# Kernel tuning notes

Measured on AMD Instinct MI355X. Metric: run time of the kernel, lower is better.

Reference implementation:

```python
import jax, jax.numpy as jnp
import numpy as np

NUM_HEADS = 16
D_IN = 1024
D_OUT = 64  # = D_IN // NUM_HEADS
N = 2048


def setup_inputs() -> dict:
    key = jax.random.key(0)
    kx, kq, kk, kv, ko = jax.random.split(key, 5)
    x = jax.random.normal(kx, (N, D_IN), dtype=jnp.float32)
    # per-head projection weights, stacked over heads (torch code keeps a
    # Python list of SelfAttention modules; stacking is the vectorized form)
    q_proj = jax.random.normal(kq, (NUM_HEADS, D_IN, D_OUT), dtype=jnp.float32)
    k_proj = jax.random.normal(kk, (NUM_HEADS, D_IN, D_OUT), dtype=jnp.float32)
    v_proj = jax.random.normal(kv, (NUM_HEADS, D_IN, D_OUT), dtype=jnp.float32)
    o_proj = jax.random.normal(ko, (D_IN, D_IN), dtype=jnp.float32)
    return {"x": x, "q_proj": q_proj, "k_proj": k_proj, "v_proj": v_proj, "o_proj": o_proj}


def reference(x, q_proj, k_proj, v_proj, o_proj):
    d_out = q_proj.shape[-1]
    # per-head projections: [H, N, E]
    q = jnp.einsum('nd,hde->hne', x, q_proj)
    k = jnp.einsum('nd,hde->hne', x, k_proj)
    v = jnp.einsum('nd,hde->hne', x, v_proj)
    # full NxN scores per head (matches the naive torch implementation's math)
    scores = jnp.einsum('hne,hme->hnm', q, k) / jnp.sqrt(jnp.float32(d_out))
    attn = jax.nn.softmax(scores, axis=-1)
    ctx = jnp.einsum('hnm,hme->hne', attn, v)
    # concat heads along the feature dim (head 0 first, as in torch.cat)
    h, n, e = ctx.shape
    out = jnp.transpose(ctx, (1, 0, 2)).reshape(n, h * e)
    return out @ o_proj
```

## Files before the change

kernel.cpp:

```cpp
#include <hip/hip_runtime.h>

#define H 16
#define N 2048
#define E 64
#define D 1024

typedef __attribute__((ext_vector_type(8))) short bf16x8;
typedef __attribute__((ext_vector_type(4))) float f32x4;

__device__ __forceinline__ float bf2f(unsigned short u) {
    union { unsigned int i; float f; } v;
    v.i = ((unsigned int)u) << 16;
    return v.f;
}
__device__ __forceinline__ unsigned short f2bf(float f) {
    unsigned int u = __float_as_uint(f);
    return (unsigned short)((u + 0x7fffu + ((u >> 16) & 1u)) >> 16);
}
#define MFMA(a, b, c) __builtin_amdgcn_mfma_f32_16x16x32_bf16(a, b, c, 0, 0, 0)

typedef __attribute__((address_space(3))) unsigned int lds_u32;
typedef const __attribute__((address_space(1))) unsigned int glb_u32;
__device__ __forceinline__ void dma16(const unsigned short* g, unsigned short* l) {
    __builtin_amdgcn_global_load_lds((glb_u32*)g, (lds_u32*)l, 16, 0, 0);
}

__device__ __forceinline__ int sw8(int row, int c)  { return row * 64  + ((c ^ (row & 7)) << 3); }
__device__ __forceinline__ int sw16(int row, int c) { return row * 128 + ((c ^ (row & 7)) << 3); }
__device__ __forceinline__ int swp(int row, int c)  { return row * 128 + ((c ^ (row & 15)) << 3); }

__global__ __launch_bounds__(256) void convert_all_kernel(
    const float* __restrict__ x,
    const float* __restrict__ qw, const float* __restrict__ kw,
    const float* __restrict__ vw, const float* __restrict__ ow,
    unsigned short* __restrict__ xh, unsigned short* __restrict__ xl,
    unsigned short* __restrict__ wBh, unsigned short* __restrict__ wBl,
    unsigned short* __restrict__ wvt, unsigned short* __restrict__ woh)
{
    __shared__ float ts[64][65];
    const int b0 = blockIdx.x;
    const int t = threadIdx.x;
    if (b0 < 2048) {
        const int i = (b0 * 256 + t) * 4;
        const float4 v = *(const float4*)&x[i];
        ushort4 hh, ll;
        hh.x = f2bf(v.x); ll.x = f2bf(v.x - bf2f(hh.x));
        hh.y = f2bf(v.y); ll.y = f2bf(v.y - bf2f(hh.y));
        hh.z = f2bf(v.z); ll.z = f2bf(v.z - bf2f(hh.z));
        hh.w = f2bf(v.w); ll.w = f2bf(v.w - bf2f(hh.w));
        *(ushort4*)&xh[i] = hh;
        *(ushort4*)&xl[i] = ll;
        return;
    }
    const int b = b0 - 2048;
    const float* src;
    int rs, dt, orow0;
    bool has_lo;
    unsigned short *dh, *dl;
    if (b < 768) {
        const int which = b >> 8, r = b & 255, h = r >> 4;
        dt = r & 15;
        src = (which == 0 ? qw : which == 1 ? kw : vw) + ((size_t)h * D + dt * 64) * E;
        rs = E;
        if (which == 0)      { dh = wBh; dl = wBl; orow0 = h * 64;        has_lo = true; }
        else if (which == 1) { dh = wBh; dl = wBl; orow0 = 1024 + h * 64; has_lo = true; }
        else                 { dh = wvt; dl = wBl; orow0 = h * 64;        has_lo = false; }
    } else {
        const int r = b - 768, ct = r >> 4;
        dt = r & 15;
        src = ow + (size_t)(dt * 64) * D + ct * 64;
        rs = D;
        orow0 = ct * 64;
        dh = woh; dl = wBl; has_lo = false;
    }
    {
        const int row = t >> 2, cb = (t & 3) * 16;
        #pragma unroll
        for (int j = 0; j < 16; j += 4) {
            const float4 v = *(const float4*)&src[row * rs + cb + j];
            ts[row][cb + j + 0] = v.x;
            ts[row][cb + j + 1] = v.y;
            ts[row][cb + j + 2] = v.z;
            ts[row][cb + j + 3] = v.w;
        }
    }
    __syncthreads();
    {
        const int cl = t >> 2, dp = (t & 3) * 16;
        bf16x8 hv0, hv1, lv0, lv1;
        #pragma unroll
        for (int i = 0; i < 16; ++i) {
            const float f = ts[dp + i][cl];
            const unsigned short hh = f2bf(f);
            const unsigned short lo = f2bf(f - bf2f(hh));
            if (i < 8) { hv0[i] = (short)hh; lv0[i] = (short)lo; }
            else       { hv1[i - 8] = (short)hh; lv1[i - 8] = (short)lo; }
        }
        const size_t o = (size_t)(orow0 + cl) * D + dt * 64 + dp;
        *(bf16x8*)&dh[o] = hv0;
        *(bf16x8*)&dh[o + 8] = hv1;
        if (has_lo) {
            *(bf16x8*)&dl[o] = lv0;
            *(bf16x8*)&dl[o + 8] = lv1;
        }
    }
}

__global__ __launch_bounds__(256, 3) void qkv_kernel(
    const unsigned short* __restrict__ xh, const unsigned short* __restrict__ xl,
    const unsigned short* __restrict__ wBh, const unsigned short* __restrict__ wBl,
    const unsigned short* __restrict__ wvt,
    unsigned short* __restrict__ Qh, unsigned short* __restrict__ Ql,
    unsigned short* __restrict__ Kh, unsigned short* __restrict__ Kl,
    unsigned short* __restrict__ Vt)
{
    __shared__ unsigned short ash[128 * 64], asl[128 * 64];
    __shared__ unsigned short bsh[64 * 64], bsl[64 * 64];
    const int n0 = blockIdx.x * 128;
    const int ct0 = blockIdx.y;
    const int sec = ct0 >> 4;
    const int hh = ct0 & 15;
    const bool isv = (sec == 2);
    const unsigned short* Bh = isv ? wvt : wBh;
    const size_t brow0 = (sec == 1 ? 1024 : 0) + hh * 64;

    const int t = threadIdx.x;
    const int lane = t & 63, wvi = t >> 6, quad = lane >> 4, l15 = lane & 15;

    f32x4 acc[2][4];
    #pragma unroll
    for (int i = 0; i < 2; ++i)
        #pragma unroll
        for (int j = 0; j < 4; ++j) acc[i][j] = (f32x4){0.f, 0.f, 0.f, 0.f};

    for (int k0 = 0; k0 < D; k0 += 64) {
        __syncthreads();
        #pragma unroll
        for (int p = 0; p < 4; ++p) {
            const int row = p * 32 + wvi * 8 + (lane >> 3);
            const int lc = (lane & 7) ^ (row & 7);
            const int lo = p * 2048 + wvi * 512 + lane * 8;
            const size_t ga = (size_t)(n0 + row) * D + k0 + lc * 8;
            dma16(&xh[ga], &ash[lo]);
            if (!isv) dma16(&xl[ga], &asl[lo]);
        }
        #pragma unroll
        for (int p = 0; p < 2; ++p) {
            const int row = p * 32 + wvi * 8 + (lane >> 3);
            const int lc = (lane & 7) ^ (row & 7);
            const int lo = p * 2048 + wvi * 512 + lane * 8;
            const size_t gb = (brow0 + row) * D + k0 + lc * 8;
            dma16(&Bh[gb], &bsh[lo]);
            if (!isv) dma16(&wBl[gb], &bsl[lo]);
        }
        __syncthreads();

        #pragma unroll
        for (int kwi = 0; kwi < 2; ++kwi) {
            const int c = kwi * 4 + quad;
            bf16x8 ah[2], al[2], bh[4], bl[4];
            #pragma unroll
            for (int i = 0; i < 2; ++i) {
                ah[i] = *(const bf16x8*)&ash[sw8(wvi * 32 + i * 16 + l15, c)];
                if (!isv) al[i] = *(const bf16x8*)&asl[sw8(wvi * 32 + i * 16 + l15, c)];
            }
            #pragma unroll
            for (int j = 0; j < 4; ++j) {
                bh[j] = *(const bf16x8*)&bsh[sw8(j * 16 + l15, c)];
                if (!isv) bl[j] = *(const bf16x8*)&bsl[sw8(j * 16 + l15, c)];
            }
            #pragma unroll
            for (int i = 0; i < 2; ++i)
                #pragma unroll
                for (int j = 0; j < 4; ++j) {
                    acc[i][j] = MFMA(ah[i], bh[j], acc[i][j]);
                    if (!isv) {
                        acc[i][j] = MFMA(ah[i], bl[j], acc[i][j]);
                        acc[i][j] = MFMA(al[i], bh[j], acc[i][j]);
                    }
                }
        }
    }

    if (isv) {
        #pragma unroll
        for (int j = 0; j < 4; ++j) {
            const int e = j * 16 + l15;
            #pragma unroll
            for (int i = 0; i < 2; ++i) {
                const int nb = n0 + wvi * 32 + i * 16 + quad * 4;
                ushort4 pk;
                pk.x = f2bf(acc[i][j][0]);
                pk.y = f2bf(acc[i][j][1]);
                pk.z = f2bf(acc[i][j][2]);
                pk.w = f2bf(acc[i][j][3]);
                *(ushort4*)&Vt[((size_t)hh * 64 + e) * N + nb] = pk;
            }
        }
    } else {
        const float scale = (sec == 0) ? 0.125f : 1.0f;
        unsigned short* Oh = (sec == 0) ? Qh : Kh;
        unsigned short* Ol = (sec == 0) ? Ql : Kl;
        #pragma unroll
        for (int j = 0; j < 4; ++j) {
            const int e = j * 16 + l15;
            #pragma unroll
            for (int i = 0; i < 2; ++i)
                #pragma unroll
                for (int r = 0; r < 4; ++r) {
                    const int n = n0 + wvi * 32 + i * 16 + quad * 4 + r;
                    const float val = acc[i][j][r] * scale;
                    const unsigned short hv = f2bf(val);
                    Oh[((size_t)hh * N + n) * E + e] = hv;
                    Ol[((size_t)hh * N + n) * E + e] = f2bf(val - bf2f(hv));
                }
        }
    }
}

__global__ __launch_bounds__(256, 2) void attn_kernel(
    const unsigned short* __restrict__ Qh, const unsigned short* __restrict__ Ql,
    const unsigned short* __restrict__ Kh, const unsigned short* __restrict__ Kl,
    const unsigned short* __restrict__ Vt,
    unsigned short* __restrict__ Op0, unsigned short* __restrict__ Op1,
    float* __restrict__ mlp)
{
    __shared__ unsigned short kbuf[2 * 16384];
    __shared__ unsigned short vts[64 * 128];
    const int r0 = blockIdx.x * 128, h = blockIdx.y, split = blockIdx.z;
    const int mb = split * 1024;
    const int t = threadIdx.x, lane = t & 63, wvi = t >> 6, quad = lane >> 4, l15 = lane & 15;

    bf16x8 qfh[2][2], qfl[2][2];
    #pragma unroll
    for (int i = 0; i < 2; ++i) {
        const size_t base = ((size_t)h * N + r0 + wvi * 32 + i * 16 + l15) * E;
        #pragma unroll
        for (int kwi = 0; kwi < 2; ++kwi) {
            qfh[i][kwi] = *(const bf16x8*)&Qh[base + kwi * 32 + quad * 8];
            qfl[i][kwi] = *(const bf16x8*)&Ql[base + kwi * 32 + quad * 8];
        }
    }

    f32x4 oacc[2][4];
    float mrow[2][4], lrow[2][4];
    #pragma unroll
    for (int i = 0; i < 2; ++i)
        #pragma unroll
        for (int j = 0; j < 4; ++j) {
            oacc[i][j] = (f32x4){0.f, 0.f, 0.f, 0.f};
            mrow[i][j] = -1e30f;
            lrow[i][j] = 0.f;
        }

    #pragma unroll
    for (int p = 0; p < 4; ++p) {
        const int row = p * 32 + wvi * 8 + (lane >> 3);
        const int lc = (lane & 7) ^ (row & 7);
        const int lo = p * 2048 + wvi * 512 + lane * 8;
        const size_t gk = ((size_t)h * N + mb + row) * E + lc * 8;
        dma16(&Kh[gk], &kbuf[lo]);
        dma16(&Kl[gk], &kbuf[8192 + lo]);
    }

    for (int it = 0; it < 8; ++it) {
        const int cur = it & 1;
        __syncthreads();

        #pragma unroll
        for (int p = 0; p < 4; ++p) {
            const int row = p * 16 + wvi * 4 + (lane >> 4);
            const int lc = (lane & 15) ^ (row & 7);
            const int lo = p * 2048 + wvi * 512 + lane * 8;
            dma16(&Vt[((size_t)h * 64 + row) * N + mb + it * 128 + lc * 8], &vts[lo]);
        }

        const unsigned short* ksh = &kbuf[cur * 16384];
        const unsigned short* ksl = ksh + 8192;

        f32x4 s[2][8];
        #pragma unroll
        for (int i = 0; i < 2; ++i)
            #pragma unroll
            for (int ct = 0; ct < 8; ++ct) s[i][ct] = (f32x4){0.f, 0.f, 0.f, 0.f};

        #pragma unroll
        for (int kwi = 0; kwi < 2; ++kwi) {
            const int c = kwi * 4 + quad;
            #pragma unroll
            for (int ct = 0; ct < 8; ++ct) {
                const bf16x8 bh = *(const bf16x8*)&ksh[sw8(ct * 16 + l15, c)];
                const bf16x8 bl = *(const bf16x8*)&ksl[sw8(ct * 16 + l15, c)];
                #pragma unroll
                for (int i = 0; i < 2; ++i) {
                    s[i][ct] = MFMA(qfh[i][kwi], bh, s[i][ct]);
                    s[i][ct] = MFMA(qfh[i][kwi], bl, s[i][ct]);
                    s[i][ct] = MFMA(qfl[i][kwi], bh, s[i][ct]);
                }
            }
        }

        #pragma unroll
        for (int i = 0; i < 2; ++i)
            #pragma unroll
            for (int r = 0; r < 4; ++r) {
                float mx = s[i][0][r];
                #pragma unroll
                for (int ct = 1; ct < 8; ++ct) mx = fmaxf(mx, s[i][ct][r]);
                mx = fmaxf(mx, __shfl_xor(mx, 1));
                mx = fmaxf(mx, __shfl_xor(mx, 2));
                mx = fmaxf(mx, __shfl_xor(mx, 4));
                mx = fmaxf(mx, __shfl_xor(mx, 8));
                const float mn = fmaxf(mrow[i][r], mx);
                const float alpha = __expf(mrow[i][r] - mn);
                mrow[i][r] = mn;
                float sum = 0.f;
                #pragma unroll
                for (int ct = 0; ct < 8; ++ct) {
                    const float p = __expf(s[i][ct][r] - mn);
                    s[i][ct][r] = p;
                    sum += p;
                }
                sum += __shfl_xor(sum, 1);
                sum += __shfl_xor(sum, 2);
                sum += __shfl_xor(sum, 4);
                sum += __shfl_xor(sum, 8);
                lrow[i][r] = lrow[i][r] * alpha + sum;
                #pragma unroll
                for (int ct = 0; ct < 4; ++ct) oacc[i][ct][r] *= alpha;
            }

        __syncthreads();

        if (it < 7) {
            #pragma unroll
            for (int p = 0; p < 4; ++p) {
                const int row = p * 32 + wvi * 8 + (lane >> 3);
                const int lc = (lane & 7) ^ (row & 7);
                const int lo = (cur ^ 1) * 16384 + p * 2048 + wvi * 512 + lane * 8;
                const size_t gk = ((size_t)h * N + mb + (it + 1) * 128 + row) * E + lc * 8;
                dma16(&Kh[gk], &kbuf[lo]);
                dma16(&Kl[gk], &kbuf[8192 + lo]);
            }
        }

        unsigned short* ps = &kbuf[cur * 16384];
        #pragma unroll
        for (int i = 0; i < 2; ++i)
            #pragma unroll
            for (int ct = 0; ct < 8; ++ct)
                #pragma unroll
                for (int r = 0; r < 4; ++r) {
                    const int row = wvi * 32 + i * 16 + quad * 4 + r;
                    const int chunk = ct * 2 + (l15 >> 3);
                    ps[swp(row, chunk) + (l15 & 7)] = f2bf(s[i][ct][r]);
                }

        #pragma unroll
        for (int kwi = 0; kwi < 4; ++kwi) {
            bf16x8 vb[4];
            #pragma unroll
            for (int ct = 0; ct < 4; ++ct)
                vb[ct] = *(const bf16x8*)&vts[sw16(ct * 16 + l15, kwi * 4 + quad)];
            #pragma unroll
            for (int i = 0; i < 2; ++i) {
                const int prow = wvi * 32 + i * 16 + l15;
                const bf16x8 pa = *(const bf16x8*)&ps[swp(prow, kwi * 4 + quad)];
                #pragma unroll
                for (int ct = 0; ct < 4; ++ct)
                    oacc[i][ct] = MFMA(pa, vb[ct], oacc[i][ct]);
            }
        }
    }

    unsigned short* Opc = split ? Op1 : Op0;
    #pragma unroll
    for (int i = 0; i < 2; ++i)
        #pragma unroll
        for (int r = 0; r < 4; ++r) {
            const int n = r0 + wvi * 32 + i * 16 + quad * 4 + r;
            if (l15 == 0) {
                mlp[(((size_t)split * 16 + h) * 2048 + n) * 2 + 0] = mrow[i][r];
                mlp[(((size_t)split * 16 + h) * 2048 + n) * 2 + 1] = lrow[i][r];
            }
            #pragma unroll
            for (int ct = 0; ct < 4; ++ct)
                Opc[((size_t)h * 2048 + n) * 64 + ct * 16 + l15] = f2bf(oacc[i][ct][r]);
        }
}

__global__ __launch_bounds__(256) void combine_kernel(
    const unsigned short* __restrict__ Op0, const unsigned short* __restrict__ Op1,
    const float* __restrict__ mlp, unsigned short* __restrict__ Ch)
{
    const int h = blockIdx.y;
    const int n = blockIdx.x * 64 + (threadIdx.x >> 2);
    const int e0 = (threadIdx.x & 3) * 16;
    const float m0 = mlp[((size_t)h * 2048 + n) * 2 + 0];
    const float l0 = mlp[((size_t)h * 2048 + n) * 2 + 1];
    const float m1 = mlp[((size_t)(16 + h) * 2048 + n) * 2 + 0];
    const float l1 = mlp[((size_t)(16 + h) * 2048 + n) * 2 + 1];
    const float M = fmaxf(m0, m1);
    const float a0 = __expf(m0 - M), a1 = __expf(m1 - M);
    const float inv = 1.f / (l0 * a0 + l1 * a1);
    const size_t ib = ((size_t)h * 2048 + n) * 64 + e0;
    const size_t ob = (size_t)n * D + h * 64 + e0;
    #pragma unroll
    for (int j = 0; j < 2; ++j) {
        const bf16x8 v0 = *(const bf16x8*)&Op0[ib + j * 8];
        const bf16x8 v1 = *(const bf16x8*)&Op1[ib + j * 8];
        bf16x8 o;
        #pragma unroll
        for (int k = 0; k < 8; ++k) {
            const float c = (bf2f((unsigned short)v0[k]) * a0 +
                             bf2f((unsigned short)v1[k]) * a1) * inv;
            o[k] = (short)f2bf(c);
        }
        *(bf16x8*)&Ch[ob + j * 8] = o;
    }
}

__global__ __launch_bounds__(256, 4) void out_proj_kernel(
    const unsigned short* __restrict__ Chh, const unsigned short* __restrict__ Wh,
    float* __restrict__ out)
{
    __shared__ unsigned short ash[64 * 64], bsh[64 * 64];
    const int n0 = blockIdx.x * 64, c0 = blockIdx.y * 64;
    const int t = threadIdx.x, lane = t & 63, wvi = t >> 6, quad = lane >> 4, l15 = lane & 15;

    f32x4 acc[4];
    #pragma unroll
    for (int j = 0; j < 4; ++j) acc[j] = (f32x4){0.f, 0.f, 0.f, 0.f};

    for (int k0 = 0; k0 < D; k0 += 64) {
        __syncthreads();
        #pragma unroll
        for (int p = 0; p < 2; ++p) {
            const int row = p * 32 + wvi * 8 + (lane >> 3);
            const int lc = (lane & 7) ^ (row & 7);
            const int lo = p * 2048 + wvi * 512 + lane * 8;
            dma16(&Chh[(size_t)(n0 + row) * D + k0 + lc * 8], &ash[lo]);
            dma16(&Wh[(size_t)(c0 + row) * D + k0 + lc * 8], &bsh[lo]);
        }
        __syncthreads();

        #pragma unroll
        for (int kwi = 0; kwi < 2; ++kwi) {
            const int c = kwi * 4 + quad;
            const bf16x8 ah = *(const bf16x8*)&ash[sw8(wvi * 16 + l15, c)];
            #pragma unroll
            for (int j = 0; j < 4; ++j) {
                const bf16x8 bh = *(const bf16x8*)&bsh[sw8(j * 16 + l15, c)];
                acc[j] = MFMA(ah, bh, acc[j]);
            }
        }
    }

    #pragma unroll
    for (int r = 0; r < 4; ++r) {
        const int n = n0 + wvi * 16 + quad * 4 + r;
        #pragma unroll
        for (int j = 0; j < 4; ++j)
            out[(size_t)n * D + c0 + j * 16 + l15] = acc[j][r];
    }
}

extern "C" void kernel_launch(void* const* d_in, const int* in_sizes, int n_in,
                              void* d_out, int out_size, void* d_ws, size_t ws_size,
                              hipStream_t stream) {
    const float* x  = (const float*)d_in[0];
    const float* qw = (const float*)d_in[1];
    const float* kw = (const float*)d_in[2];
    const float* vw = (const float*)d_in[3];
    const float* ow = (const float*)d_in[4];
    float* out = (float*)d_out;

    unsigned short* ws = (unsigned short*)d_ws;
    const size_t M1 = 1024 * 1024;
    unsigned short* wBh = ws;
    unsigned short* wBl = ws + 2 * M1;
    unsigned short* wvt = ws + 4 * M1;
    unsigned short* woh = ws + 5 * M1;
    unsigned short* xh  = ws + 6 * M1;
    unsigned short* xl  = ws + 8 * M1;
    unsigned short* Qh  = ws + 10 * M1;
    unsigned short* Ql  = ws + 12 * M1;
    unsigned short* Kh  = ws + 14 * M1;
    unsigned short* Kl  = ws + 16 * M1;
    unsigned short* Vt  = ws + 18 * M1;
    unsigned short* Ch  = xh;

    unsigned short* Op0 = wBh;
    unsigned short* Op1 = wBl;
    float* mlp = (float*)wvt;

    convert_all_kernel<<<3072, 256, 0, stream>>>(x, qw, kw, vw, ow,
                                                 xh, xl, wBh, wBl, wvt, woh);
    qkv_kernel<<<dim3(16, 48), 256, 0, stream>>>(xh, xl, wBh, wBl, wvt,
                                                 Qh, Ql, Kh, Kl, Vt);
    attn_kernel<<<dim3(16, 16, 2), 256, 0, stream>>>(Qh, Ql, Kh, Kl, Vt,
                                                     Op0, Op1, mlp);
    combine_kernel<<<dim3(32, 16), 256, 0, stream>>>(Op0, Op1, mlp, Ch);
    out_proj_kernel<<<dim3(32, 16), 256, 0, stream>>>(Ch, woh, out);
}
```

Baseline: 181.2 us.

## Transpose score MFMA so P stays in registers for PV product

Swaps MFMA operand order so the score tile comes out transposed, with each lane holding one query row across four keys. The probabilities can then be packed straight into bf16 B-operands with v_cvt_pk_bf16_f32, which removes the P write to and read from LDS. Softmax reductions become per-lane with two cross-quad shuffles instead of four, and V is loaded through registers then stored into LDS instead of DMA. This cuts LDS traffic and shuffles, at the cost of more register pressure and synchronous global loads for V.

```diff
diff --git a/kernel.cpp b/kernel.cpp
--- a/kernel.cpp
+++ b/kernel.cpp
@@ -7,6 +7,7 @@
 
 typedef __attribute__((ext_vector_type(8))) short bf16x8;
 typedef __attribute__((ext_vector_type(4))) float f32x4;
+typedef __attribute__((ext_vector_type(4))) unsigned int u32x4;
 
 __device__ __forceinline__ float bf2f(unsigned short u) {
     union { unsigned int i; float f; } v;
@@ -17,6 +18,17 @@
     unsigned int u = __float_as_uint(f);
     return (unsigned short)((u + 0x7fffu + ((u >> 16) & 1u)) >> 16);
 }
+__device__ __forceinline__ unsigned int cvtpk(float lo, float hi) {
+    unsigned int r;
+    asm("v_cvt_pk_bf16_f32 %0, %1, %2" : "=v"(r) : "v"(lo), "v"(hi));
+    return r;
+}
+__device__ __forceinline__ bf16x8 pk4(unsigned int a, unsigned int b,
+                                      unsigned int c, unsigned int d) {
+    union { u32x4 u; bf16x8 h; } x;
+    x.u = (u32x4){a, b, c, d};
+    return x.h;
+}
 #define MFMA(a, b, c) __builtin_amdgcn_mfma_f32_16x16x32_bf16(a, b, c, 0, 0, 0)
 
 typedef __attribute__((address_space(3))) unsigned int lds_u32;
@@ -26,8 +38,6 @@
 }
 
 __device__ __forceinline__ int sw8(int row, int c)  { return row * 64  + ((c ^ (row & 7)) << 3); }
-__device__ __forceinline__ int sw16(int row, int c) { return row * 128 + ((c ^ (row & 7)) << 3); }
-__device__ __forceinline__ int swp(int row, int c)  { return row * 128 + ((c ^ (row & 15)) << 3); }
 
 __global__ __launch_bounds__(256) void convert_all_kernel(
     const float* __restrict__ x,
@@ -243,15 +253,14 @@
     }
 
     f32x4 oacc[2][4];
-    float mrow[2][4], lrow[2][4];
+    float mrow[2] = {-1e30f, -1e30f}, lrow[2] = {0.f, 0.f};
     #pragma unroll
     for (int i = 0; i < 2; ++i)
         #pragma unroll
-        for (int j = 0; j < 4; ++j) {
-            oacc[i][j] = (f32x4){0.f, 0.f, 0.f, 0.f};
-            mrow[i][j] = -1e30f;
-            lrow[i][j] = 0.f;
-        }
+        for (int j = 0; j < 4; ++j) oacc[i][j] = (f32x4){0.f, 0.f, 0.f, 0.f};
+
+    const int ve = wvi * 16 + (lane >> 2);
+    const int vc = lane & 3;
 
     #pragma unroll
     for (int p = 0; p < 4; ++p) {
@@ -266,13 +275,14 @@
     for (int it = 0; it < 8; ++it) {
         const int cur = it & 1;
         __syncthreads();
-
-        #pragma unroll
-        for (int p = 0; p < 4; ++p) {
-            const int row = p * 16 + wvi * 4 + (lane >> 4);
-            const int lc = (lane & 15) ^ (row & 7);
-            const int lo = p * 2048 + wvi * 512 + lane * 8;
-            dma16(&Vt[((size_t)h * 64 + row) * N + mb + it * 128 + lc * 8], &vts[lo]);
+        const int mcol = mb + it * 128;
+
+        uint2 vr0[4], vr1[4];
+        #pragma unroll
+        for (int z = 0; z < 4; ++z) {
+            const size_t gb = ((size_t)h * 64 + ve) * N + mcol + vc * 32 + z * 4;
+            vr0[z] = *(const uint2*)&Vt[gb];
+            vr1[z] = *(const uint2*)&Vt[gb + 16];
         }
 
         const unsigned short* ksh = &kbuf[cur * 16384];
@@ -289,47 +299,59 @@
             const int c = kwi * 4 + quad;
             #pragma unroll
             for (int ct = 0; ct < 8; ++ct) {
-                const bf16x8 bh = *(const bf16x8*)&ksh[sw8(ct * 16 + l15, c)];
-                const bf16x8 bl = *(const bf16x8*)&ksl[sw8(ct * 16 + l15, c)];
+                const bf16x8 kh = *(const bf16x8*)&ksh[sw8(ct * 16 + l15, c)];
+                const bf16x8 kl = *(const bf16x8*)&ksl[sw8(ct * 16 + l15, c)];
                 #pragma unroll
                 for (int i = 0; i < 2; ++i) {
-                    s[i][ct] = MFMA(qfh[i][kwi], bh, s[i][ct]);
-                    s[i][ct] = MFMA(qfh[i][kwi], bl, s[i][ct]);
-                    s[i][ct] = MFMA(qfl[i][kwi], bh, s[i][ct]);
+                    s[i][ct] = MFMA(kh, qfh[i][kwi], s[i][ct]);
+                    s[i][ct] = MFMA(kl, qfh[i][kwi], s[i][ct]);
+                    s[i][ct] = MFMA(kh, qfl[i][kwi], s[i][ct]);
                 }
             }
         }
 
         #pragma unroll
-        for (int i = 0; i < 2; ++i)
-            #pragma unroll
-            for (int r = 0; r < 4; ++r) {
-                float mx = s[i][0][r];
-                #pragma unroll
-                for (int ct = 1; ct < 8; ++ct) mx = fmaxf(mx, s[i][ct][r]);
-                mx = fmaxf(mx, __shfl_xor(mx, 1));
-                mx = fmaxf(mx, __shfl_xor(mx, 2));
-                mx = fmaxf(mx, __shfl_xor(mx, 4));
-                mx = fmaxf(mx, __shfl_xor(mx, 8));
-                const float mn = fmaxf(mrow[i][r], mx);
-                const float alpha = __expf(mrow[i][r] - mn);
-                mrow[i][r] = mn;
-                float sum = 0.f;
-                #pragma unroll
-                for (int ct = 0; ct < 8; ++ct) {
-                    const float p = __expf(s[i][ct][r] - mn);
-                    s[i][ct][r] = p;
-                    sum += p;
-                }
-                sum += __shfl_xor(sum, 1);
-                sum += __shfl_xor(sum, 2);
-                sum += __shfl_xor(sum, 4);
-                sum += __shfl_xor(sum, 8);
-                lrow[i][r] = lrow[i][r] * alpha + sum;
-                #pragma unroll
-                for (int ct = 0; ct < 4; ++ct) oacc[i][ct][r] *= alpha;
-            }
-
+        for (int i = 0; i < 2; ++i) {
+            float m0 = s[i][0][0], m1 = s[i][0][1], m2 = s[i][0][2], m3 = s[i][0][3];
+            #pragma unroll
+            for (int ct = 1; ct < 8; ++ct) {
+                m0 = fmaxf(m0, s[i][ct][0]); m1 = fmaxf(m1, s[i][ct][1]);
+                m2 = fmaxf(m2, s[i][ct][2]); m3 = fmaxf(m3, s[i][ct][3]);
+            }
+            float mx = fmaxf(fmaxf(m0, m1), fmaxf(m2, m3));
+            mx = fmaxf(mx, __shfl_xor(mx, 16));
+            mx = fmaxf(mx, __shfl_xor(mx, 32));
+            const float mn = fmaxf(mrow[i], mx);
+            const float al = __expf(mrow[i] - mn);
+            mrow[i] = mn;
+            float s0 = 0.f, s1 = 0.f, s2 = 0.f, s3 = 0.f;
+            #pragma unroll
+            for (int ct = 0; ct < 8; ++ct) {
+                const float p0 = __expf(s[i][ct][0] - mn);
+                const float p1 = __expf(s[i][ct][1] - mn);
+                const float p2 = __expf(s[i][ct][2] - mn);
+                const float p3 = __expf(s[i][ct][3] - mn);
+                s[i][ct][0] = p0; s[i][ct][1] = p1;
+                s[i][ct][2] = p2; s[i][ct][3] = p3;
+                s0 += p0; s1 += p1; s2 += p2; s3 += p3;
+            }
+            float sum = (s0 + s1) + (s2 + s3);
+            sum += __shfl_xor(sum, 16);
+            sum += __shfl_xor(sum, 32);
+            lrow[i] = lrow[i] * al + sum;
+            #pragma unroll
+            for (int ct = 0; ct < 4; ++ct) {
+                oacc[i][ct][0] *= al; oacc[i][ct][1] *= al;
+                oacc[i][ct][2] *= al; oacc[i][ct][3] *= al;
+            }
+        }
+
+        #pragma unroll
+        for (int z = 0; z < 4; ++z) {
+            const int c16 = vc * 4 + z;
+            u32x4 w = (u32x4){vr0[z].x, vr0[z].y, vr1[z].x, vr1[z].y};
+            *(u32x4*)&vts[ve * 128 + ((c16 ^ (ve & 7)) << 3)] = w;
+        }
         __syncthreads();
 
         if (it < 7) {
@@ -338,55 +360,51 @@
                 const int row = p * 32 + wvi * 8 + (lane >> 3);
                 const int lc = (lane & 7) ^ (row & 7);
                 const int lo = (cur ^ 1) * 16384 + p * 2048 + wvi * 512 + lane * 8;
-                const size_t gk = ((size_t)h * N + mb + (it + 1) * 128 + row) * E + lc * 8;
+                const size_t gk = ((size_t)h * N + mcol + 128 + row) * E + lc * 8;
                 dma16(&Kh[gk], &kbuf[lo]);
                 dma16(&Kl[gk], &kbuf[8192 + lo]);
             }
         }
 
-        unsigned short* ps = &kbuf[cur * 16384];
-        #pragma unroll
-        for (int i = 0; i < 2; ++i)
-            #pragma unroll
-            for (int ct = 0; ct < 8; ++ct)
+        #pragma unroll
+        for (int kb = 0; kb < 4; ++kb) {
+            bf16x8 pb[2];
+            #pragma unroll
+            for (int i = 0; i < 2; ++i)
+                pb[i] = pk4(cvtpk(s[i][2 * kb][0],     s[i][2 * kb][1]),
+                            cvtpk(s[i][2 * kb][2],     s[i][2 * kb][3]),
+                            cvtpk(s[i][2 * kb + 1][0], s[i][2 * kb + 1][1]),
+                            cvtpk(s[i][2 * kb + 1][2], s[i][2 * kb + 1][3]));
+            #pragma unroll
+            for (int ct = 0; ct < 4; ++ct) {
+                const int re = ct * 16 + l15;
+                const bf16x8 va =
+                    *(const bf16x8*)&vts[re * 128 + (((kb * 4 + quad) ^ (re & 7)) << 3)];
                 #pragma unroll
-                for (int r = 0; r < 4; ++r) {
-                    const int row = wvi * 32 + i * 16 + quad * 4 + r;
-                    const int chunk = ct * 2 + (l15 >> 3);
-                    ps[swp(row, chunk) + (l15 & 7)] = f2bf(s[i][ct][r]);
-                }
-
-        #pragma unroll
-        for (int kwi = 0; kwi < 4; ++kwi) {
-            bf16x8 vb[4];
-            #pragma unroll
-            for (int ct = 0; ct < 4; ++ct)
-                vb[ct] = *(const bf16x8*)&vts[sw16(ct * 16 + l15, kwi * 4 + quad)];
-            #pragma unroll
-            for (int i = 0; i < 2; ++i) {
-                const int prow = wvi * 32 + i * 16 + l15;
-                const bf16x8 pa = *(const bf16x8*)&ps[swp(prow, kwi * 4 + quad)];
-                #pragma unroll
-                for (int ct = 0; ct < 4; ++ct)
-                    oacc[i][ct] = MFMA(pa, vb[ct], oacc[i][ct]);
+                for (int i = 0; i < 2; ++i)
+                    oacc[i][ct] = MFMA(va, pb[i], oacc[i][ct]);
             }
         }
     }
 
     unsigned short* Opc = split ? Op1 : Op0;
     #pragma unroll
-    for (int i = 0; i < 2; ++i)
-        #pragma unroll
-        for (int r = 0; r < 4; ++r) {
-            const int n = r0 + wvi * 32 + i * 16 + quad * 4 + r;
-            if (l15 == 0) {
-                mlp[(((size_t)split * 16 + h) * 2048 + n) * 2 + 0] = mrow[i][r];
-                mlp[(((size_t)split * 16 + h) * 2048 + n) * 2 + 1] = lrow[i][r];
-            }
-            #pragma unroll
-            for (int ct = 0; ct < 4; ++ct)
-                Opc[((size_t)h * 2048 + n) * 64 + ct * 16 + l15] = f2bf(oacc[i][ct][r]);
-        }
+    for (int i = 0; i < 2; ++i) {
+        const int n = r0 + wvi * 32 + i * 16 + l15;
+        if (quad == 0) {
+            mlp[(((size_t)split * 16 + h) * 2048 + n) * 2 + 0] = mrow[i];
+            mlp[(((size_t)split * 16 + h) * 2048 + n) * 2 + 1] = lrow[i];
+        }
+        #pragma unroll
+        for (int ct = 0; ct < 4; ++ct) {
+            ushort4 pk;
+            pk.x = f2bf(oacc[i][ct][0]);
+            pk.y = f2bf(oacc[i][ct][1]);
+            pk.z = f2bf(oacc[i][ct][2]);
+            pk.w = f2bf(oacc[i][ct][3]);
+            *(ushort4*)&Opc[((size_t)h * 2048 + n) * 64 + ct * 16 + quad * 4] = pk;
+        }
+    }
 }
 
 __global__ __launch_bounds__(256) void combine_kernel(
```

Result: faster. 164.3 us (-9.3%).
